# Performance work log

Measured on AMD Instinct MI355X. Metric: run time of the kernel, lower is better.

Reference implementation:

```python
import jax, jax.numpy as jnp
import numpy as np

NUM_BLOCKS = 32
B, S = 8, 2048


def setup_inputs() -> dict:
    key = jax.random.key(0)
    k1, k2, k3 = jax.random.split(key, 3)
    h = jax.random.uniform(k1, (B, S, NUM_BLOCKS, 4), dtype=jnp.float32)
    W = jax.random.uniform(k2, (B, S, NUM_BLOCKS, NUM_BLOCKS), dtype=jnp.float32)
    stim = jax.random.uniform(k3, (B, S, NUM_BLOCKS), dtype=jnp.float32)
    return {"h": h, "W": W, "stim": stim}


def _step(h, W, stim):
    nb = h.shape[-2]
    eye = jnp.eye(nb, dtype=W.dtype)
    W_no_self = W * (1.0 - eye)                      # zero self-connections
    # neighbor inflow: [b,s,i,j] @ [b,s,j,c] -> [b,s,i,c]
    inflow = jnp.einsum('bsij,bsjc->bsic', W_no_self, h)
    total_w = W_no_self.sum(axis=-1, keepdims=True) + 1e-8
    neigh = inflow / total_w                          # weighted neighbor mean

    E, P, G, L = h[..., 0], h[..., 1], h[..., 2], h[..., 3]
    En, Pn, Gn, Ln = neigh[..., 0], neigh[..., 1], neigh[..., 2], neigh[..., 3]

    clamp01 = lambda x: jnp.clip(x, 0.0, 1.0)
    E_new = clamp01(E + 0.3 * stim - 0.4 * P - 0.2 * G)
    P_new = clamp01(P + 0.5 * stim + 0.3 * (Pn - P) - 0.2 * E)
    G_new = clamp01(G + 0.4 * E * (1.0 - P) + 0.2 * (Gn - G) - 0.3 * P)
    good_neighbor = 0.5 * En + 0.5 * Gn
    L_new = clamp01(L + 0.4 * good_neighbor + 0.3 * (Ln - L) - 0.3 * P)

    h_new = jnp.stack([E_new, P_new, G_new, L_new], axis=-1)  # [b,s,nb,4]

    # pairwise euclidean distance over the 4 EPGL channels (torch.cdist p=2)
    diff = h_new[..., :, None, :] - h_new[..., None, :, :]    # [b,s,nb,nb,4]
    sq = jnp.sum(diff * diff, axis=-1)
    # safe sqrt: zero distance -> 0 (matches cdist; avoids nan grads)
    h_diff = jnp.where(sq > 0, jnp.sqrt(jnp.where(sq > 0, sq, 1.0)), 0.0)

    mutual_L = 0.5 * (L_new[..., :, None] + L_new[..., None, :])
    alpha, beta = 0.1 * mutual_L, 0.05
    W_new = W + alpha * h_diff - beta * W
    W_new = jnp.clip(W_new, 0.0, 1.0) * (1.0 - eye)
    return h_new, W_new


def reference(h, W, stim):
    return _step(h, W, stim)
```

## Files before the change

kernel.cpp:

```cpp
#include <hip/hip_runtime.h>

#define NB 32
#define WAVES_PER_BLOCK 4

__device__ __forceinline__ float clamp01(float x) {
    return fminf(fmaxf(x, 0.0f), 1.0f);
}

__global__ __launch_bounds__(256, 4) void biotoken_step(
    const float* __restrict__ h,
    const float* __restrict__ W,
    const float* __restrict__ stim,
    float* __restrict__ out_h,
    float* __restrict__ out_W)
{
    const int lw    = threadIdx.x & 63;
    const int wave  = threadIdx.x >> 6;
    const int token = blockIdx.x * WAVES_PER_BLOCK + wave;

    __shared__ float s_hin [WAVES_PER_BLOCK][NB * 4];
    __shared__ float s_hnew[WAVES_PER_BLOCK][NB * 4];
    __shared__ float s_stim[WAVES_PER_BLOCK][NB];
    __shared__ float s_W   [WAVES_PER_BLOCK][NB * 33];

    const float4* Wt = (const float4*)(W + (size_t)token * (NB * NB));
    const float4* ht = (const float4*)(h + (size_t)token * (NB * 4));
    const float*  st = stim + (size_t)token * NB;

    float4 wr[4];
    wr[0] = Wt[0 * 64 + lw];
    wr[1] = Wt[1 * 64 + lw];
    wr[2] = Wt[2 * 64 + lw];
    wr[3] = Wt[3 * 64 + lw];

    if (lw < NB) {
        ((float4*)s_hin[wave])[lw] = ht[lw];
        s_stim[wave][lw] = st[lw];
    }

    {
        float* sw = s_W[wave];
        const int g = lw >> 3;
        const int c = (lw & 7) * 4;
        #pragma unroll
        for (int k = 0; k < 4; ++k) {
            const int r = k * 8 + g;
            const float* wp = (const float*)&wr[k];
            sw[r * 33 + c + 0] = wp[0];
            sw[r * 33 + c + 1] = wp[1];
            sw[r * 33 + c + 2] = wp[2];
            sw[r * 33 + c + 3] = wp[3];
        }
    }
    __syncthreads();

    const int i    = lw & 31;
    const int half = lw >> 5;
    const float* sw   = s_W[wave];
    const float* shin = s_hin[wave];

    float accE = 0.f, accP = 0.f, accG = 0.f, accL = 0.f, tot = 0.f;
    #pragma unroll
    for (int t = 0; t < 16; ++t) {
        const int j = half * 16 + t;
        float w = sw[i * 33 + j];
        w = (j == i) ? 0.0f : w;
        const float4 hj = *(const float4*)&shin[j * 4];
        accE = fmaf(w, hj.x, accE);
        accP = fmaf(w, hj.y, accP);
        accG = fmaf(w, hj.z, accG);
        accL = fmaf(w, hj.w, accL);
        tot += w;
    }
    accE += __shfl_xor(accE, 32);
    accP += __shfl_xor(accP, 32);
    accG += __shfl_xor(accG, 32);
    accL += __shfl_xor(accL, 32);
    tot  += __shfl_xor(tot,  32);

    const float inv = 1.0f / (tot + 1e-8f);
    const float En = accE * inv, Pn = accP * inv, Gn = accG * inv, Ln = accL * inv;

    const float4 hi = *(const float4*)&shin[i * 4];
    const float E = hi.x, P = hi.y, G = hi.z, L = hi.w;
    const float sti = s_stim[wave][i];

    const float E_new = clamp01(E + 0.3f * sti - 0.4f * P - 0.2f * G);
    const float P_new = clamp01(P + 0.5f * sti + 0.3f * (Pn - P) - 0.2f * E);
    const float G_new = clamp01(G + 0.4f * E * (1.0f - P) + 0.2f * (Gn - G) - 0.3f * P);
    const float good  = 0.5f * En + 0.5f * Gn;
    const float L_new = clamp01(L + 0.4f * good + 0.3f * (Ln - L) - 0.3f * P);

    if (half == 0) {
        const float4 hn = make_float4(E_new, P_new, G_new, L_new);
        ((float4*)s_hnew[wave])[i] = hn;
        ((float4*)(out_h + (size_t)token * (NB * 4)))[i] = hn;
    }
    __syncthreads();

    const float* shn = s_hnew[wave];
    float4* outWt = (float4*)(out_W + (size_t)token * (NB * NB));

    const int jb0 = (lw & 7) * 4;
    float4 hjv[4];
    #pragma unroll
    for (int e = 0; e < 4; ++e) {
        hjv[e] = *(const float4*)&shn[(jb0 + e) * 4];
    }

    #pragma unroll
    for (int k = 0; k < 4; ++k) {
        const int m  = k * 64 + lw;
        const int r  = m >> 3;
        const float4 hr = *(const float4*)&shn[r * 4];
        const float  Lr = hr.w;
        const float* wp = (const float*)&wr[k];
        float4 res;
        float* resp = &res.x;
        #pragma unroll
        for (int e = 0; e < 4; ++e) {
            const int j = jb0 + e;
            const float4 hj = hjv[e];
            const float dx = hr.x - hj.x;
            const float dy = hr.y - hj.y;
            const float dz = hr.z - hj.z;
            const float dw = hr.w - hj.w;
            const float sq = dx * dx + dy * dy + dz * dz + dw * dw;
            const float dist = sqrtf(sq);
            const float mutual = 0.5f * (Lr + hj.w);
            float wn = 0.95f * wp[e] + 0.1f * mutual * dist;
            wn = clamp01(wn);
            resp[e] = (j == r) ? 0.0f : wn;
        }
        outWt[m] = res;
    }
}

extern "C" void kernel_launch(void* const* d_in, const int* in_sizes, int n_in,
                              void* d_out, int out_size, void* d_ws, size_t ws_size,
                              hipStream_t stream) {
    const float* h    = (const float*)d_in[0];
    const float* W    = (const float*)d_in[1];
    const float* stim = (const float*)d_in[2];

    const int tokens = in_sizes[2] / NB;
    float* out_h = (float*)d_out;
    float* out_W = (float*)d_out + (size_t)tokens * NB * 4;

    const int blocks = tokens / WAVES_PER_BLOCK;
    biotoken_step<<<blocks, 256, 0, stream>>>(h, W, stim, out_h, out_W);
}
```

Measured before the change: 135.6 us.

## Compute neighbor inflow from register W tile with shuffle reductions, drop LDS W staging

Each lane now computes partial inflow sums directly from the W float4 values it already holds in registers, reducing across the 8 lanes of a row with xor shuffles instead of staging W through a padded shared-memory tile. Each lane also keeps the new h values for its own rows in registers for the W update, and the launch-bounds occupancy hint rises from 4 to 8 blocks. This removes the 16 KB per-block LDS tile and its write/read traffic and raises occupancy for this memory-bound kernel. In exchange it adds shuffle instructions and some redundant per-row h updates, plus register pressure under the tighter bound.

```diff
diff --git a/kernel.cpp b/kernel.cpp
--- a/kernel.cpp
+++ b/kernel.cpp
@@ -7,7 +7,7 @@
     return fminf(fmaxf(x, 0.0f), 1.0f);
 }
 
-__global__ __launch_bounds__(256, 4) void biotoken_step(
+__global__ __launch_bounds__(256, 8) void biotoken_step(
     const float* __restrict__ h,
     const float* __restrict__ W,
     const float* __restrict__ stim,
@@ -17,11 +17,12 @@
     const int lw    = threadIdx.x & 63;
     const int wave  = threadIdx.x >> 6;
     const int token = blockIdx.x * WAVES_PER_BLOCK + wave;
+    const int g     = lw >> 3;
+    const int c     = lw & 7;
 
     __shared__ float s_hin [WAVES_PER_BLOCK][NB * 4];
     __shared__ float s_hnew[WAVES_PER_BLOCK][NB * 4];
     __shared__ float s_stim[WAVES_PER_BLOCK][NB];
-    __shared__ float s_W   [WAVES_PER_BLOCK][NB * 33];
 
     const float4* Wt = (const float4*)(W + (size_t)token * (NB * NB));
     const float4* ht = (const float4*)(h + (size_t)token * (NB * 4));
@@ -37,90 +38,92 @@
         ((float4*)s_hin[wave])[lw] = ht[lw];
         s_stim[wave][lw] = st[lw];
     }
+    __syncthreads();
 
-    {
-        float* sw = s_W[wave];
-        const int g = lw >> 3;
-        const int c = (lw & 7) * 4;
+    const float* shin = s_hin[wave];
+
+    const float4 hj0 = ((const float4*)shin)[4 * c + 0];
+    const float4 hj1 = ((const float4*)shin)[4 * c + 1];
+    const float4 hj2 = ((const float4*)shin)[4 * c + 2];
+    const float4 hj3 = ((const float4*)shin)[4 * c + 3];
+
+    float aE[4], aP[4], aG[4], aL[4], aT[4];
+    #pragma unroll
+    for (int k = 0; k < 4; ++k) {
+        const int r = k * 8 + g;
+        const float* wp = (const float*)&wr[k];
+        const float w0 = (4 * c + 0 == r) ? 0.0f : wp[0];
+        const float w1 = (4 * c + 1 == r) ? 0.0f : wp[1];
+        const float w2 = (4 * c + 2 == r) ? 0.0f : wp[2];
+        const float w3 = (4 * c + 3 == r) ? 0.0f : wp[3];
+        aE[k] = fmaf(w3, hj3.x, fmaf(w2, hj2.x, fmaf(w1, hj1.x, w0 * hj0.x)));
+        aP[k] = fmaf(w3, hj3.y, fmaf(w2, hj2.y, fmaf(w1, hj1.y, w0 * hj0.y)));
+        aG[k] = fmaf(w3, hj3.z, fmaf(w2, hj2.z, fmaf(w1, hj1.z, w0 * hj0.z)));
+        aL[k] = fmaf(w3, hj3.w, fmaf(w2, hj2.w, fmaf(w1, hj1.w, w0 * hj0.w)));
+        aT[k] = (w0 + w1) + (w2 + w3);
+    }
+
+    #pragma unroll
+    for (int m = 1; m <= 4; m <<= 1) {
         #pragma unroll
         for (int k = 0; k < 4; ++k) {
-            const int r = k * 8 + g;
-            const float* wp = (const float*)&wr[k];
-            sw[r * 33 + c + 0] = wp[0];
-            sw[r * 33 + c + 1] = wp[1];
-            sw[r * 33 + c + 2] = wp[2];
-            sw[r * 33 + c + 3] = wp[3];
+            aE[k] += __shfl_xor(aE[k], m);
+            aP[k] += __shfl_xor(aP[k], m);
+            aG[k] += __shfl_xor(aG[k], m);
+            aL[k] += __shfl_xor(aL[k], m);
+            aT[k] += __shfl_xor(aT[k], m);
         }
     }
-    __syncthreads();
 
-    const int i    = lw & 31;
-    const int half = lw >> 5;
-    const float* sw   = s_W[wave];
-    const float* shin = s_hin[wave];
+    float4 hn[4];
+    #pragma unroll
+    for (int k = 0; k < 4; ++k) {
+        const int r = k * 8 + g;
+        const float4 hi = ((const float4*)shin)[r];
+        const float sti = s_stim[wave][r];
+        const float inv = 1.0f / (aT[k] + 1e-8f);
+        const float En = aE[k] * inv, Pn = aP[k] * inv;
+        const float Gn = aG[k] * inv, Ln = aL[k] * inv;
+        const float E = hi.x, P = hi.y, G = hi.z, L = hi.w;
 
-    float accE = 0.f, accP = 0.f, accG = 0.f, accL = 0.f, tot = 0.f;
-    #pragma unroll
-    for (int t = 0; t < 16; ++t) {
-        const int j = half * 16 + t;
-        float w = sw[i * 33 + j];
-        w = (j == i) ? 0.0f : w;
-        const float4 hj = *(const float4*)&shin[j * 4];
-        accE = fmaf(w, hj.x, accE);
-        accP = fmaf(w, hj.y, accP);
-        accG = fmaf(w, hj.z, accG);
-        accL = fmaf(w, hj.w, accL);
-        tot += w;
+        const float E_new = clamp01(E + 0.3f * sti - 0.4f * P - 0.2f * G);
+        const float P_new = clamp01(P + 0.5f * sti + 0.3f * (Pn - P) - 0.2f * E);
+        const float G_new = clamp01(G + 0.4f * E * (1.0f - P) + 0.2f * (Gn - G) - 0.3f * P);
+        const float good  = 0.5f * En + 0.5f * Gn;
+        const float L_new = clamp01(L + 0.4f * good + 0.3f * (Ln - L) - 0.3f * P);
+        hn[k] = make_float4(E_new, P_new, G_new, L_new);
     }
-    accE += __shfl_xor(accE, 32);
-    accP += __shfl_xor(accP, 32);
-    accG += __shfl_xor(accG, 32);
-    accL += __shfl_xor(accL, 32);
-    tot  += __shfl_xor(tot,  32);
 
-    const float inv = 1.0f / (tot + 1e-8f);
-    const float En = accE * inv, Pn = accP * inv, Gn = accG * inv, Ln = accL * inv;
-
-    const float4 hi = *(const float4*)&shin[i * 4];
-    const float E = hi.x, P = hi.y, G = hi.z, L = hi.w;
-    const float sti = s_stim[wave][i];
-
-    const float E_new = clamp01(E + 0.3f * sti - 0.4f * P - 0.2f * G);
-    const float P_new = clamp01(P + 0.5f * sti + 0.3f * (Pn - P) - 0.2f * E);
-    const float G_new = clamp01(G + 0.4f * E * (1.0f - P) + 0.2f * (Gn - G) - 0.3f * P);
-    const float good  = 0.5f * En + 0.5f * Gn;
-    const float L_new = clamp01(L + 0.4f * good + 0.3f * (Ln - L) - 0.3f * P);
-
-    if (half == 0) {
-        const float4 hn = make_float4(E_new, P_new, G_new, L_new);
-        ((float4*)s_hnew[wave])[i] = hn;
-        ((float4*)(out_h + (size_t)token * (NB * 4)))[i] = hn;
+    if (c < 4) {
+        const float4 a   = (c & 1) ? hn[1] : hn[0];
+        const float4 b   = (c & 1) ? hn[3] : hn[2];
+        const float4 sel = (c & 2) ? b : a;
+        const int r = c * 8 + g;
+        ((float4*)s_hnew[wave])[r] = sel;
+        ((float4*)(out_h + (size_t)token * (NB * 4)))[r] = sel;
     }
     __syncthreads();
 
     const float* shn = s_hnew[wave];
+    const float4 qj0 = ((const float4*)shn)[4 * c + 0];
+    const float4 qj1 = ((const float4*)shn)[4 * c + 1];
+    const float4 qj2 = ((const float4*)shn)[4 * c + 2];
+    const float4 qj3 = ((const float4*)shn)[4 * c + 3];
+
     float4* outWt = (float4*)(out_W + (size_t)token * (NB * NB));
-
-    const int jb0 = (lw & 7) * 4;
-    float4 hjv[4];
-    #pragma unroll
-    for (int e = 0; e < 4; ++e) {
-        hjv[e] = *(const float4*)&shn[(jb0 + e) * 4];
-    }
-
     #pragma unroll
     for (int k = 0; k < 4; ++k) {
-        const int m  = k * 64 + lw;
-        const int r  = m >> 3;
-        const float4 hr = *(const float4*)&shn[r * 4];
+        const int r  = k * 8 + g;
+        const float4 hr = hn[k];
         const float  Lr = hr.w;
         const float* wp = (const float*)&wr[k];
         float4 res;
         float* resp = &res.x;
+        const float4 qj[4] = { qj0, qj1, qj2, qj3 };
         #pragma unroll
         for (int e = 0; e < 4; ++e) {
-            const int j = jb0 + e;
-            const float4 hj = hjv[e];
+            const int j = 4 * c + e;
+            const float4 hj = qj[e];
             const float dx = hr.x - hj.x;
             const float dy = hr.y - hj.y;
             const float dz = hr.z - hj.z;
@@ -132,7 +135,7 @@
             wn = clamp01(wn);
             resp[e] = (j == r) ? 0.0f : wn;
         }
-        outWt[m] = res;
+        outWt[k * 64 + lw] = res;
     }
 }
 
```

New measurement: 155.6 us. 14.7% more time.

## Double-buffer tokens per wave with async global-to-LDS loads

Applied to the files above, without the earlier changes.

Each wave now processes four tokens in sequence. It uses global_load_lds to stage the next token's W and h directly into a second LDS buffer while the current token is computed, which is meant to hide global-load latency. The padded-row transpose is replaced by an unpadded layout read with a rotated index, so bank conflicts are avoided without it. The grid shrinks by four, which may reduce the number of waves available for latency hiding, and LDS use per block grows to roughly 36KB, which may lower occupancy. The block-wide __syncthreads at the top of each iteration stands in for a proper wait on the async loads.

```diff
diff --git a/kernel.cpp b/kernel.cpp
--- a/kernel.cpp
+++ b/kernel.cpp
@@ -2,9 +2,35 @@
 
 #define NB 32
 #define WAVES_PER_BLOCK 4
+#define TOKENS_PER_WAVE 4
 
 __device__ __forceinline__ float clamp01(float x) {
     return fminf(fmaxf(x, 0.0f), 1.0f);
+}
+
+__device__ __forceinline__ void gload_lds16(const float* g, float* lds) {
+    __builtin_amdgcn_global_load_lds(
+        (const __attribute__((address_space(1))) void*)g,
+        (__attribute__((address_space(3))) void*)lds, 16, 0, 0);
+}
+__device__ __forceinline__ void gload_lds4(const float* g, float* lds) {
+    __builtin_amdgcn_global_load_lds(
+        (const __attribute__((address_space(1))) void*)g,
+        (__attribute__((address_space(3))) void*)lds, 4, 0, 0);
+}
+
+__device__ __forceinline__ void stage_token(
+    const float* __restrict__ W, const float* __restrict__ h,
+    int token, float* bufW, float* bufH, int lw)
+{
+    const float* Wt = W + (size_t)token * (NB * NB);
+    #pragma unroll
+    for (int k = 0; k < 4; ++k) {
+        gload_lds16(Wt + (size_t)(k * 64 + lw) * 4, bufW + k * 256);
+    }
+    const float* ht = h + (size_t)token * (NB * 4);
+    gload_lds4(ht + lw,      bufH);
+    gload_lds4(ht + 64 + lw, bufH + 64);
 }
 
 __global__ __launch_bounds__(256, 4) void biotoken_step(
@@ -14,125 +40,114 @@
     float* __restrict__ out_h,
     float* __restrict__ out_W)
 {
-    const int lw    = threadIdx.x & 63;
-    const int wave  = threadIdx.x >> 6;
-    const int token = blockIdx.x * WAVES_PER_BLOCK + wave;
+    const int lw   = threadIdx.x & 63;
+    const int wave = threadIdx.x >> 6;
+    const int tok0 = (blockIdx.x * WAVES_PER_BLOCK + wave) * TOKENS_PER_WAVE;
+    const int i    = lw & 31;
+    const int half = lw >> 5;
 
-    __shared__ float s_hin [WAVES_PER_BLOCK][NB * 4];
+    __shared__ float s_W   [WAVES_PER_BLOCK][2][NB * NB];
+    __shared__ float s_hin [WAVES_PER_BLOCK][2][NB * 4];
     __shared__ float s_hnew[WAVES_PER_BLOCK][NB * 4];
-    __shared__ float s_stim[WAVES_PER_BLOCK][NB];
-    __shared__ float s_W   [WAVES_PER_BLOCK][NB * 33];
 
-    const float4* Wt = (const float4*)(W + (size_t)token * (NB * NB));
-    const float4* ht = (const float4*)(h + (size_t)token * (NB * 4));
-    const float*  st = stim + (size_t)token * NB;
+    stage_token(W, h, tok0, s_W[wave][0], s_hin[wave][0], lw);
+    float stiC = stim[(size_t)tok0 * NB + i];
+    float stiN = 0.0f;
 
-    float4 wr[4];
-    wr[0] = Wt[0 * 64 + lw];
-    wr[1] = Wt[1 * 64 + lw];
-    wr[2] = Wt[2 * 64 + lw];
-    wr[3] = Wt[3 * 64 + lw];
+    #pragma unroll
+    for (int tt = 0; tt < TOKENS_PER_WAVE; ++tt) {
+        const int cur   = tt & 1;
+        const int token = tok0 + tt;
 
-    if (lw < NB) {
-        ((float4*)s_hin[wave])[lw] = ht[lw];
-        s_stim[wave][lw] = st[lw];
-    }
+        __syncthreads();
 
-    {
-        float* sw = s_W[wave];
-        const int g = lw >> 3;
-        const int c = (lw & 7) * 4;
+        if (tt + 1 < TOKENS_PER_WAVE) {
+            stage_token(W, h, token + 1, s_W[wave][cur ^ 1],
+                        s_hin[wave][cur ^ 1], lw);
+            stiN = stim[(size_t)(token + 1) * NB + i];
+        }
+
+        const float* bw   = s_W[wave][cur];
+        const float* shin = s_hin[wave][cur];
+
+        float accE = 0.f, accP = 0.f, accG = 0.f, accL = 0.f, tot = 0.f;
+        #pragma unroll
+        for (int t = 0; t < 16; ++t) {
+            const int jj = (half << 4) | ((t + i) & 15);
+            float w = bw[i * 32 + jj];
+            w = (jj == i) ? 0.0f : w;
+            const float4 hj = *(const float4*)&shin[jj * 4];
+            accE = fmaf(w, hj.x, accE);
+            accP = fmaf(w, hj.y, accP);
+            accG = fmaf(w, hj.z, accG);
+            accL = fmaf(w, hj.w, accL);
+            tot += w;
+        }
+        accE += __shfl_xor(accE, 32);
+        accP += __shfl_xor(accP, 32);
+        accG += __shfl_xor(accG, 32);
+        accL += __shfl_xor(accL, 32);
+        tot  += __shfl_xor(tot,  32);
+
+        const float inv = 1.0f / (tot + 1e-8f);
+        const float En = accE * inv, Pn = accP * inv;
+        const float Gn = accG * inv, Ln = accL * inv;
+
+        const float4 hi = *(const float4*)&shin[i * 4];
+        const float E = hi.x, P = hi.y, G = hi.z, L = hi.w;
+
+        const float E_new = clamp01(E + 0.3f * stiC - 0.4f * P - 0.2f * G);
+        const float P_new = clamp01(P + 0.5f * stiC + 0.3f * (Pn - P) - 0.2f * E);
+        const float G_new = clamp01(G + 0.4f * E * (1.0f - P) + 0.2f * (Gn - G) - 0.3f * P);
+        const float good  = 0.5f * En + 0.5f * Gn;
+        const float L_new = clamp01(L + 0.4f * good + 0.3f * (Ln - L) - 0.3f * P);
+
+        if (half == 0) {
+            const float4 hn = make_float4(E_new, P_new, G_new, L_new);
+            ((float4*)s_hnew[wave])[i] = hn;
+            ((float4*)(out_h + (size_t)token * (NB * 4)))[i] = hn;
+        }
+        __builtin_amdgcn_wave_barrier();
+
+        const float* shn = s_hnew[wave];
+        float4* outWt = (float4*)(out_W + (size_t)token * (NB * NB));
+
+        const int jb0 = (lw & 7) * 4;
+        float4 hjv[4];
+        #pragma unroll
+        for (int e = 0; e < 4; ++e) {
+            hjv[e] = *(const float4*)&shn[(jb0 + e) * 4];
+        }
+
         #pragma unroll
         for (int k = 0; k < 4; ++k) {
-            const int r = k * 8 + g;
-            const float* wp = (const float*)&wr[k];
-            sw[r * 33 + c + 0] = wp[0];
-            sw[r * 33 + c + 1] = wp[1];
-            sw[r * 33 + c + 2] = wp[2];
-            sw[r * 33 + c + 3] = wp[3];
+            const int m = k * 64 + lw;
+            const int r = m >> 3;
+            const float4 wv = *(const float4*)&bw[(size_t)m * 4];
+            const float4 hr = *(const float4*)&shn[r * 4];
+            const float  Lr = hr.w;
+            const float* wp = (const float*)&wv;
+            float4 res;
+            float* resp = &res.x;
+            #pragma unroll
+            for (int e = 0; e < 4; ++e) {
+                const int j = jb0 + e;
+                const float4 hj = hjv[e];
+                const float dx = hr.x - hj.x;
+                const float dy = hr.y - hj.y;
+                const float dz = hr.z - hj.z;
+                const float dw = hr.w - hj.w;
+                const float sq = dx * dx + dy * dy + dz * dz + dw * dw;
+                const float dist = sqrtf(sq);
+                const float mutual = 0.5f * (Lr + hj.w);
+                float wn = 0.95f * wp[e] + 0.1f * mutual * dist;
+                wn = clamp01(wn);
+                resp[e] = (j == r) ? 0.0f : wn;
+            }
+            outWt[m] = res;
         }
-    }
-    __syncthreads();
 
-    const int i    = lw & 31;
-    const int half = lw >> 5;
-    const float* sw   = s_W[wave];
-    const float* shin = s_hin[wave];
-
-    float accE = 0.f, accP = 0.f, accG = 0.f, accL = 0.f, tot = 0.f;
-    #pragma unroll
-    for (int t = 0; t < 16; ++t) {
-        const int j = half * 16 + t;
-        float w = sw[i * 33 + j];
-        w = (j == i) ? 0.0f : w;
-        const float4 hj = *(const float4*)&shin[j * 4];
-        accE = fmaf(w, hj.x, accE);
-        accP = fmaf(w, hj.y, accP);
-        accG = fmaf(w, hj.z, accG);
-        accL = fmaf(w, hj.w, accL);
-        tot += w;
-    }
-    accE += __shfl_xor(accE, 32);
-    accP += __shfl_xor(accP, 32);
-    accG += __shfl_xor(accG, 32);
-    accL += __shfl_xor(accL, 32);
-    tot  += __shfl_xor(tot,  32);
-
-    const float inv = 1.0f / (tot + 1e-8f);
-    const float En = accE * inv, Pn = accP * inv, Gn = accG * inv, Ln = accL * inv;
-
-    const float4 hi = *(const float4*)&shin[i * 4];
-    const float E = hi.x, P = hi.y, G = hi.z, L = hi.w;
-    const float sti = s_stim[wave][i];
-
-    const float E_new = clamp01(E + 0.3f * sti - 0.4f * P - 0.2f * G);
-    const float P_new = clamp01(P + 0.5f * sti + 0.3f * (Pn - P) - 0.2f * E);
-    const float G_new = clamp01(G + 0.4f * E * (1.0f - P) + 0.2f * (Gn - G) - 0.3f * P);
-    const float good  = 0.5f * En + 0.5f * Gn;
-    const float L_new = clamp01(L + 0.4f * good + 0.3f * (Ln - L) - 0.3f * P);
-
-    if (half == 0) {
-        const float4 hn = make_float4(E_new, P_new, G_new, L_new);
-        ((float4*)s_hnew[wave])[i] = hn;
-        ((float4*)(out_h + (size_t)token * (NB * 4)))[i] = hn;
-    }
-    __syncthreads();
-
-    const float* shn = s_hnew[wave];
-    float4* outWt = (float4*)(out_W + (size_t)token * (NB * NB));
-
-    const int jb0 = (lw & 7) * 4;
-    float4 hjv[4];
-    #pragma unroll
-    for (int e = 0; e < 4; ++e) {
-        hjv[e] = *(const float4*)&shn[(jb0 + e) * 4];
-    }
-
-    #pragma unroll
-    for (int k = 0; k < 4; ++k) {
-        const int m  = k * 64 + lw;
-        const int r  = m >> 3;
-        const float4 hr = *(const float4*)&shn[r * 4];
-        const float  Lr = hr.w;
-        const float* wp = (const float*)&wr[k];
-        float4 res;
-        float* resp = &res.x;
-        #pragma unroll
-        for (int e = 0; e < 4; ++e) {
-            const int j = jb0 + e;
-            const float4 hj = hjv[e];
-            const float dx = hr.x - hj.x;
-            const float dy = hr.y - hj.y;
-            const float dz = hr.z - hj.z;
-            const float dw = hr.w - hj.w;
-            const float sq = dx * dx + dy * dy + dz * dz + dw * dw;
-            const float dist = sqrtf(sq);
-            const float mutual = 0.5f * (Lr + hj.w);
-            float wn = 0.95f * wp[e] + 0.1f * mutual * dist;
-            wn = clamp01(wn);
-            resp[e] = (j == r) ? 0.0f : wn;
-        }
-        outWt[m] = res;
+        stiC = stiN;
     }
 }
 
@@ -147,6 +162,6 @@
     float* out_h = (float*)d_out;
     float* out_W = (float*)d_out + (size_t)tokens * NB * 4;
 
-    const int blocks = tokens / WAVES_PER_BLOCK;
+    const int blocks = tokens / (WAVES_PER_BLOCK * TOKENS_PER_WAVE);
     biotoken_step<<<blocks, 256, 0, stream>>>(h, W, stim, out_h, out_W);
 }
```

After: 138.4 us. 2.1% more time.
